# Performance work log

Hardware: AMD Instinct MI355X
Metric: run time of the kernel (lower is better)

## Reference

```python
import jax, jax.numpy as jnp
import numpy as np

N = 1024          # num_nodes
E = 16384         # num_edges (avg degree 16)
D = 256           # in_channels
P = 2.0           # PairwiseDistance p
SELF_ADD = 0.5
UPPER_BOUND = 2.0
# scores lie in [SELF_ADD, 1+SELF_ADD] = [0.5, 1.5], so the greedy loop adds
# at most ceil(UPPER_BOUND / 0.5) = 4 edges; 6 masked steps is a safe bound.
MAX_STEPS = 6


def setup_inputs() -> dict:
    key = jax.random.key(0)
    k1, k2 = jax.random.split(key)
    x = jax.random.normal(k1, (N, D), dtype=jnp.float32)
    edge_index = jax.random.randint(k2, (2, E), 0, N, dtype=jnp.int64)
    return {"x": x, "edge_index": edge_index}


def _edge_scores(x, src, dst):
    # compute_distance_score: L2 pairwise distance, min-max normalized, + self_add
    diff = x[src] - x[dst]                      # [E, D]
    dist = jnp.sqrt(jnp.sum(diff * diff, axis=-1))
    dist = (dist - dist.min()) / (dist.max() - dist.min())
    return dist + SELF_ADD                      # [E]


def _search_all(edge_score, src, dst):
    # Vectorized version of node__cluster_search: for each seed node i, greedily
    # add the min-score edge leaving the cluster until total score >= UPPER_BOUND
    # or no frontier edge exists. Fixed-length masked scan == original while-loop.
    def search(i):
        inc = jnp.zeros((N,), bool).at[i].set(True)      # in_cluster mask
        row = jnp.zeros((N,), jnp.float32)               # node_score_matrix row
        tot = jnp.float32(0.0)

        def step(state, _):
            inc, row, tot = state
            valid = inc[src] & ~inc[dst]                 # frontier edges [E]
            active = (tot < UPPER_BOUND) & jnp.any(valid)
            masked = jnp.where(valid, edge_score, jnp.inf)
            e = jnp.argmin(masked)                       # min-score frontier edge
            s = edge_score[e]
            u, v = src[e], dst[e]
            inc2 = inc.at[v].set(True)
            row2 = row.at[u].add(s * 0.5).at[v].add(s * 0.5)
            inc = jnp.where(active, inc2, inc)
            row = jnp.where(active, row2, row)
            tot = jnp.where(active, tot + s, tot)
            return (inc, row, tot), None

        (inc, row, tot), _ = jax.lax.scan(step, (inc, row, tot), None, length=MAX_STEPS)
        return inc.astype(jnp.float32), row

    return jax.vmap(search)(jnp.arange(N))


def _keep_first_unique_rows(assign):
    # np.unique(..., axis=0) dedup, shape-static variant: keep first occurrence of
    # each distinct binary row, zero out duplicates. Double random-hash row compare.
    rng = np.random.default_rng(12345)
    r1 = jnp.asarray(rng.integers(1, 2**20, size=(N,)), dtype=jnp.int32)
    r2 = jnp.asarray(rng.integers(1, 2**20, size=(N,)), dtype=jnp.int32)
    ai = assign.astype(jnp.int32)
    h1, h2 = ai @ r1, ai @ r2
    eq = (h1[:, None] == h1[None, :]) & (h2[:, None] == h2[None, :])  # [N, N]
    dup = jnp.any(jnp.tril(eq, k=-1), axis=1)
    return (~dup).astype(jnp.float32)


def reference(x, edge_index):
    src, dst = edge_index[0], edge_index[1]
    edge_score = _edge_scores(x, src, dst)
    assign, nsm = _search_all(edge_score, src, dst)      # [N, N], [N, N]

    keep = _keep_first_unique_rows(assign)               # [N]
    assign_k = assign * keep[:, None]
    nsm_k = nsm * keep[:, None]

    # dense adjacency (to_dense_adj), pooled adjacency, binarize, drop self-loops
    adj = jnp.zeros((N, N), jnp.float32).at[src, dst].add(1.0)
    adj_new = assign_k @ adj @ assign_k.T
    adj_new = (adj_new > 0).astype(jnp.float32) * (1.0 - jnp.eye(N, dtype=jnp.float32))

    x_new = nsm_k @ x                                    # pooled features [N, D]
    return adj_new, x_new, assign_k, nsm_k
```

## Files before the change

### kernel.cpp

```cpp
#include <hip/hip_runtime.h>
#include <cstdint>

#define NN 1024
#define NE 16384
#define DF 256
#define UB 2.0f
#define MAXSEL 6
#define CAP 128
#define NB2 1024
#define DSTR 16

typedef unsigned long long u64;

__global__ void k_zero(uint4* __restrict__ p) {
    p[blockIdx.x * 256 + threadIdx.x] = make_uint4(0, 0, 0, 0);
}

__global__ void k_dist_build(const float* __restrict__ x, const int* __restrict__ src,
                             const int* __restrict__ dst, int* __restrict__ deg,
                             u64* __restrict__ slots,
                             uint32_t* __restrict__ pmin, uint32_t* __restrict__ pmax) {
    __shared__ uint32_t smin[4], smax[4];
    int t = threadIdx.x;
    int wid = t >> 6, lane = t & 63;
    int c16 = lane & 15;
    int e = blockIdx.x * 16 + wid * 4 + (lane >> 4);
    int u = src[e], v = dst[e];
    const float4* xa = (const float4*)(x + (size_t)u * DF);
    const float4* xb = (const float4*)(x + (size_t)v * DF);
    float4 a0 = xa[c16],      b0 = xb[c16];
    float4 a1 = xa[c16 + 16], b1 = xb[c16 + 16];
    float4 a2 = xa[c16 + 32], b2 = xb[c16 + 32];
    float4 a3 = xa[c16 + 48], b3 = xb[c16 + 48];
    double s = 0.0;
    {
        float d;
        d = a0.x-b0.x; s += (double)d*d;  d = a0.y-b0.y; s += (double)d*d;
        d = a0.z-b0.z; s += (double)d*d;  d = a0.w-b0.w; s += (double)d*d;
        d = a1.x-b1.x; s += (double)d*d;  d = a1.y-b1.y; s += (double)d*d;
        d = a1.z-b1.z; s += (double)d*d;  d = a1.w-b1.w; s += (double)d*d;
        d = a2.x-b2.x; s += (double)d*d;  d = a2.y-b2.y; s += (double)d*d;
        d = a2.z-b2.z; s += (double)d*d;  d = a2.w-b2.w; s += (double)d*d;
        d = a3.x-b3.x; s += (double)d*d;  d = a3.y-b3.y; s += (double)d*d;
        d = a3.z-b3.z; s += (double)d*d;  d = a3.w-b3.w; s += (double)d*d;
    }
    s += __shfl_xor(s, 1, 64);
    s += __shfl_xor(s, 2, 64);
    s += __shfl_xor(s, 4, 64);
    s += __shfl_xor(s, 8, 64);
    uint32_t db = __float_as_uint(sqrtf((float)s));
    if (c16 == 0) {
        int pos = atomicAdd(&deg[u * DSTR], 1);
        if (pos < CAP)
            slots[(size_t)u * CAP + pos] =
                ((u64)db << 24) | ((u64)(uint32_t)e << 10) | (u64)(uint32_t)v;
    }
    uint32_t mnv = db, mxv = db;
    uint32_t o;
    o = (uint32_t)__shfl_xor((int)mnv, 16, 64); mnv = min(mnv, o);
    o = (uint32_t)__shfl_xor((int)mnv, 32, 64); mnv = min(mnv, o);
    o = (uint32_t)__shfl_xor((int)mxv, 16, 64); mxv = max(mxv, o);
    o = (uint32_t)__shfl_xor((int)mxv, 32, 64); mxv = max(mxv, o);
    if (lane == 0) { smin[wid] = mnv; smax[wid] = mxv; }
    __syncthreads();
    if (t == 0) {
        pmin[blockIdx.x] = min(min(smin[0], smin[1]), min(smin[2], smin[3]));
        pmax[blockIdx.x] = max(max(smax[0], smax[1]), max(smax[2], smax[3]));
    }
}

__global__ void k_search(const int* __restrict__ deg, const u64* __restrict__ slots,
                         const uint32_t* __restrict__ pmin, const uint32_t* __restrict__ pmax,
                         const int* __restrict__ src,
                         uint32_t* __restrict__ masks, uint32_t* __restrict__ maskT,
                         int* __restrict__ selU, int* __restrict__ selV,
                         float* __restrict__ selS, int* __restrict__ selCnt,
                         u64* __restrict__ sig, u64* __restrict__ dc64) {
    __shared__ uint32_t inc[32];
    __shared__ int members[8];
    __shared__ int degL[8], offL[9];
    __shared__ float s_tot;
    __shared__ int s_nmem;
    int i = blockIdx.x, lane = threadIdx.x;
    if (lane < 32) inc[lane] = 0;

    uint32_t mnb = 0xFFFFFFFFu, mxb = 0u;
    const uint4* p4n = (const uint4*)pmin;
    const uint4* p4x = (const uint4*)pmax;
    for (int k = lane; k < NB2 / 4; k += 64) {
        uint4 a = p4n[k], b = p4x[k];
        mnb = min(mnb, min(min(a.x, a.y), min(a.z, a.w)));
        mxb = max(mxb, max(max(b.x, b.y), max(b.z, b.w)));
    }
    for (int off = 32; off; off >>= 1) {
        uint32_t oa = (uint32_t)__shfl_xor((int)mnb, off, 64);
        uint32_t ob = (uint32_t)__shfl_xor((int)mxb, off, 64);
        mnb = min(mnb, oa);
        mxb = max(mxb, ob);
    }
    float MN = __uint_as_float(mnb);
    float MX = __uint_as_float(mxb);

    if (lane == 0) {
        inc[i >> 5] = 1u << (i & 31);
        members[0] = i;
        s_tot = 0.0f;
        s_nmem = 1;
    }
    __syncthreads();
    int cnt = 0;
    for (int step = 0; step < MAXSEL; ++step) {
        if (s_tot >= UB) break;
        int nm = s_nmem;
        if (lane < nm) degL[lane] = min(deg[members[lane] * DSTR], CAP);
        __syncthreads();
        if (lane == 0) {
            offL[0] = 0;
            for (int m = 0; m < nm; ++m) offL[m + 1] = offL[m] + degL[m];
        }
        __syncthreads();
        int T = offL[nm];
        u64 best = ~0ull;
        for (int f = lane; f < T; f += 64) {
            int m = 0;
            while (f >= offL[m + 1]) ++m;
            u64 en = slots[(size_t)members[m] * CAP + (f - offL[m])];
            int v = (int)(en & 1023);
            if (!((inc[v >> 5] >> (v & 31)) & 1u) && en < best) best = en;
        }
        for (int off = 32; off; off >>= 1) {
            u64 o = __shfl_xor(best, off, 64);
            if (o < best) best = o;
        }
        if (best == ~0ull) break;
        if (lane == 0) {
            uint32_t db = (uint32_t)(best >> 24);
            int e = (int)((best >> 10) & 0x3FFF);
            int v = (int)(best & 1023);
            float dd = __uint_as_float(db);
            float s = (dd - MN) / (MX - MN) + 0.5f;
            int u = src[e];
            inc[v >> 5] |= 1u << (v & 31);
            members[s_nmem++] = v;
            selU[i * 8 + cnt] = u;
            selV[i * 8 + cnt] = v;
            selS[i * 8 + cnt] = s;
            s_tot += s;
        }
        cnt++;
        __syncthreads();
    }
    __syncthreads();
    if (lane == 0) {
        selCnt[i] = cnt;
        u64 h = 1469598103934665603ull;
        for (int w = 0; w < 32; ++w) { h ^= inc[w]; h *= 1099511628211ull; }
        sig[i] = h;
        u64 d = 0; int nc = 0;
        for (int k = 1; k < s_nmem; ++k) {
            int v = members[k];
            if (v < i) { d |= ((u64)(uint32_t)v) << (4 + 10 * nc); ++nc; }
        }
        dc64[i] = d | (u64)nc;
    }
    if (lane < 32) masks[(size_t)i * 32 + lane] = inc[lane];
    if (lane < s_nmem) {
        int n = members[lane];
        atomicOr(&maskT[(size_t)n * 32 + (i >> 5)], 1u << (i & 31));
    }
}

__global__ void k_rows(const float* __restrict__ x, const int* __restrict__ deg,
                       const u64* __restrict__ slots,
                       const uint32_t* __restrict__ masks, const uint32_t* __restrict__ maskT,
                       const u64* __restrict__ sig, const u64* __restrict__ dc64,
                       const int* __restrict__ selU, const int* __restrict__ selV,
                       const float* __restrict__ selS, const int* __restrict__ selCnt,
                       float* __restrict__ outAdj, float* __restrict__ outAs,
                       float* __restrict__ outNsm, float* __restrict__ outX) {
    __shared__ u64 sigL[NN];
    __shared__ uint32_t keepb[32];
    __shared__ uint32_t R[32], MI[32], orow[32];
    __shared__ uint32_t part[8][32];
    __shared__ int su[8], ssv[8];
    __shared__ float ss[8];
    __shared__ int s_c;
    int i = blockIdx.x, t = threadIdx.x;

    for (int j = t; j < NN; j += 256) sigL[j] = sig[j];
    if (t < 32) { keepb[t] = 0; R[t] = 0; MI[t] = masks[(size_t)i * 32 + t]; }
    if (t == 0) s_c = selCnt[i];
    if (t < 8) { su[t] = selU[i*8+t]; ssv[t] = selV[i*8+t]; ss[t] = selS[i*8+t]; }
    __syncthreads();

    for (int q = 0; q < 4; ++q) {
        int j = t + q * 256;
        u64 d = dc64[j];
        int cj = (int)(d & 15);
        u64 sj = sigL[j];
        bool dup = false;
        for (int k = 0; k < cj; ++k) {
            int v = (int)((d >> (4 + 10 * k)) & 1023);
            if (sigL[v] == sj) { dup = true; break; }
        }
        if (!dup) atomicOr(&keepb[j >> 5], 1u << (j & 31));
    }

    int c = s_c;
    for (int m = 0; m <= c; ++m) {
        int u = (m == 0) ? i : ssv[m - 1];
        int dc = min(deg[u * DSTR], CAP);
        const u64* sl = slots + (size_t)u * CAP;
        for (int k = t; k < dc; k += 256) {
            int v = (int)(sl[k] & 1023);
            atomicOr(&R[v >> 5], 1u << (v & 31));
        }
    }
    __syncthreads();
    int kp = (keepb[i >> 5] >> (i & 31)) & 1;

    int g = t >> 5, l = t & 31;
    uint32_t acc = 0;
    if (kp) {
        for (int wi = g; wi < 32; wi += 8) {
            uint32_t bits = R[wi];
            while (bits) {
                int b0 = __ffs(bits) - 1; bits &= bits - 1;
                uint32_t v0 = maskT[((size_t)(wi * 32 + b0)) * 32 + l];
                if (bits) {
                    int b1 = __ffs(bits) - 1; bits &= bits - 1;
                    v0 |= maskT[((size_t)(wi * 32 + b1)) * 32 + l];
                }
                acc |= v0;
            }
        }
    }
    part[g][l] = acc;
    __syncthreads();
    if (t < 32) {
        uint32_t o = 0;
        for (int gg = 0; gg < 8; ++gg) o |= part[gg][t];
        orow[t] = o & keepb[t];
    }
    __syncthreads();

    int j0 = t * 4;
    int w = j0 >> 5, sh = j0 & 31;
    float4 vadj = {0,0,0,0}, vas = {0,0,0,0}, vnsm = {0,0,0,0};
    if (kp) {
        uint32_t ob = orow[w] >> sh;
        uint32_t mb = MI[w] >> sh;
        vadj.x = ((ob     ) & 1) && (j0     != i) ? 1.0f : 0.0f;
        vadj.y = ((ob >> 1) & 1) && (j0 + 1 != i) ? 1.0f : 0.0f;
        vadj.z = ((ob >> 2) & 1) && (j0 + 2 != i) ? 1.0f : 0.0f;
        vadj.w = ((ob >> 3) & 1) && (j0 + 3 != i) ? 1.0f : 0.0f;
        vas.x = (mb      & 1) ? 1.0f : 0.0f;
        vas.y = ((mb>>1) & 1) ? 1.0f : 0.0f;
        vas.z = ((mb>>2) & 1) ? 1.0f : 0.0f;
        vas.w = ((mb>>3) & 1) ? 1.0f : 0.0f;
        for (int k = 0; k < c; ++k) {
            float h = ss[k] * 0.5f;
            int u = su[k], v = ssv[k];
            vnsm.x += ((u == j0    ) ? h : 0.0f) + ((v == j0    ) ? h : 0.0f);
            vnsm.y += ((u == j0 + 1) ? h : 0.0f) + ((v == j0 + 1) ? h : 0.0f);
            vnsm.z += ((u == j0 + 2) ? h : 0.0f) + ((v == j0 + 2) ? h : 0.0f);
            vnsm.w += ((u == j0 + 3) ? h : 0.0f) + ((v == j0 + 3) ? h : 0.0f);
        }
    }
    ((float4*)outAdj)[(size_t)i * (NN/4) + t] = vadj;
    ((float4*)outAs )[(size_t)i * (NN/4) + t] = vas;
    ((float4*)outNsm)[(size_t)i * (NN/4) + t] = vnsm;

    float accx = 0.0f;
    if (kp) {
        for (int k = 0; k < c; ++k) {
            float h = ss[k] * 0.5f;
            accx += h * x[(size_t)su[k] * DF + t];
            accx += h * x[(size_t)ssv[k] * DF + t];
        }
    }
    outX[(size_t)i * DF + t] = accx;
}

extern "C" void kernel_launch(void* const* d_in, const int* in_sizes, int n_in,
                              void* d_out, int out_size, void* d_ws, size_t ws_size,
                              hipStream_t stream) {
    const float* x = (const float*)d_in[0];
    const int* ei = (const int*)d_in[1];
    const int* src = ei;
    const int* dst = ei + NE;

    float* out = (float*)d_out;
    float* out_adj = out;
    float* out_x   = out + (size_t)NN * NN;
    float* out_as  = out_x + (size_t)NN * DF;
    float* out_nsm = out_as + (size_t)NN * NN;

    char* w = (char*)d_ws;
    u64*      slots = (u64*)w;       w += (size_t)NN * CAP * 8;
    u64*      sig   = (u64*)w;       w += (size_t)NN * 8;
    u64*      dc64  = (u64*)w;       w += (size_t)NN * 8;
    int*      deg   = (int*)w;       w += (size_t)NN * DSTR * 4;
    uint32_t* maskT = (uint32_t*)w;  w += (size_t)NN * 32 * 4;
    uint32_t* pmin  = (uint32_t*)w;  w += (size_t)NB2 * 4;
    uint32_t* pmax  = (uint32_t*)w;  w += (size_t)NB2 * 4;
    uint32_t* masks = (uint32_t*)w;  w += (size_t)NN * 32 * 4;
    int*      selU  = (int*)w;       w += (size_t)NN * 8 * 4;
    int*      selV  = (int*)w;       w += (size_t)NN * 8 * 4;
    float*    selS  = (float*)w;     w += (size_t)NN * 8 * 4;
    int*      selCnt= (int*)w;       w += (size_t)NN * 4;

    k_zero<<<48, 256, 0, stream>>>((uint4*)deg);
    k_dist_build<<<NB2, 256, 0, stream>>>(x, src, dst, deg, slots, pmin, pmax);
    k_search<<<NN, 64, 0, stream>>>(deg, slots, pmin, pmax, src,
                                    masks, maskT, selU, selV, selS, selCnt, sig, dc64);
    k_rows<<<NN, 256, 0, stream>>>(x, deg, slots, masks, maskT, sig, dc64,
                                   selU, selV, selS, selCnt,
                                   out_adj, out_as, out_nsm, out_x);
}
```

Before: 34.86 us.

## Use sentinel-filled fixed-width adjacency slots and cache member edges in shared memory

Adjacency slot capacity is halved and the slots are pre-filled with all-ones sentinels, so readers scan a fixed 64 entries per node and no longer need per-node degree reads or prefix offsets. The search kernel loads each newly added member's slot row once into a shared-memory pool and rescans it each step, dropping repeated global loads and two barriers per step. The rows kernel builds a compact list of reachable nodes before OR-ing maskT rows. The fill kernel now writes the whole slots array, and any node with more than 64 out-edges would silently lose edges, which is fine for average degree 16 but not guaranteed.

```diff
diff --git a/kernel.cpp b/kernel.cpp
--- a/kernel.cpp
+++ b/kernel.cpp
@@ -6,14 +6,16 @@
 #define DF 256
 #define UB 2.0f
 #define MAXSEL 6
-#define CAP 128
+#define CAP 64
 #define NB2 1024
 #define DSTR 16
+#define FILLB 176
 
 typedef unsigned long long u64;
 
-__global__ void k_zero(uint4* __restrict__ p) {
-    p[blockIdx.x * 256 + threadIdx.x] = make_uint4(0, 0, 0, 0);
+__global__ void k_fill(uint4* __restrict__ p) {
+    uint32_t v = (blockIdx.x < 128) ? 0xFFFFFFFFu : 0u;
+    p[blockIdx.x * 256 + threadIdx.x] = make_uint4(v, v, v, v);
 }
 
 __global__ void k_dist_build(const float* __restrict__ x, const int* __restrict__ src,
@@ -69,16 +71,16 @@
     }
 }
 
-__global__ void k_search(const int* __restrict__ deg, const u64* __restrict__ slots,
+__global__ void k_search(const u64* __restrict__ slots,
                          const uint32_t* __restrict__ pmin, const uint32_t* __restrict__ pmax,
                          const int* __restrict__ src,
                          uint32_t* __restrict__ masks, uint32_t* __restrict__ maskT,
                          int* __restrict__ selU, int* __restrict__ selV,
                          float* __restrict__ selS, int* __restrict__ selCnt,
                          u64* __restrict__ sig, u64* __restrict__ dc64) {
+    __shared__ u64 pool[8][64];
     __shared__ uint32_t inc[32];
     __shared__ int members[8];
-    __shared__ int degL[8], offL[9];
     __shared__ float s_tot;
     __shared__ int s_nmem;
     int i = blockIdx.x, lane = threadIdx.x;
@@ -107,26 +109,20 @@
         s_tot = 0.0f;
         s_nmem = 1;
     }
+    pool[0][lane] = slots[(size_t)i * CAP + lane];
     __syncthreads();
     int cnt = 0;
     for (int step = 0; step < MAXSEL; ++step) {
         if (s_tot >= UB) break;
         int nm = s_nmem;
-        if (lane < nm) degL[lane] = min(deg[members[lane] * DSTR], CAP);
-        __syncthreads();
-        if (lane == 0) {
-            offL[0] = 0;
-            for (int m = 0; m < nm; ++m) offL[m + 1] = offL[m] + degL[m];
-        }
-        __syncthreads();
-        int T = offL[nm];
         u64 best = ~0ull;
-        for (int f = lane; f < T; f += 64) {
-            int m = 0;
-            while (f >= offL[m + 1]) ++m;
-            u64 en = slots[(size_t)members[m] * CAP + (f - offL[m])];
-            int v = (int)(en & 1023);
-            if (!((inc[v >> 5] >> (v & 31)) & 1u) && en < best) best = en;
+        #pragma unroll
+        for (int m = 0; m < 8; ++m) {
+            if (m < nm) {
+                u64 en = pool[m][lane];
+                int v = (int)(en & 1023);
+                if (!((inc[v >> 5] >> (v & 31)) & 1u) && en < best) best = en;
+            }
         }
         for (int off = 32; off; off >>= 1) {
             u64 o = __shfl_xor(best, off, 64);
@@ -139,15 +135,17 @@
             int v = (int)(best & 1023);
             float dd = __uint_as_float(db);
             float s = (dd - MN) / (MX - MN) + 0.5f;
-            int u = src[e];
             inc[v >> 5] |= 1u << (v & 31);
             members[s_nmem++] = v;
-            selU[i * 8 + cnt] = u;
+            selU[i * 8 + cnt] = src[e];
             selV[i * 8 + cnt] = v;
             selS[i * 8 + cnt] = s;
             s_tot += s;
         }
         cnt++;
+        __syncthreads();
+        int newm = s_nmem - 1;
+        pool[newm][lane] = slots[(size_t)members[newm] * CAP + lane];
         __syncthreads();
     }
     __syncthreads();
@@ -170,8 +168,7 @@
     }
 }
 
-__global__ void k_rows(const float* __restrict__ x, const int* __restrict__ deg,
-                       const u64* __restrict__ slots,
+__global__ void k_rows(const float* __restrict__ x, const u64* __restrict__ slots,
                        const uint32_t* __restrict__ masks, const uint32_t* __restrict__ maskT,
                        const u64* __restrict__ sig, const u64* __restrict__ dc64,
                        const int* __restrict__ selU, const int* __restrict__ selV,
@@ -182,6 +179,8 @@
     __shared__ uint32_t keepb[32];
     __shared__ uint32_t R[32], MI[32], orow[32];
     __shared__ uint32_t part[8][32];
+    __shared__ int list[512];
+    __shared__ int s_lcnt;
     __shared__ int su[8], ssv[8];
     __shared__ float ss[8];
     __shared__ int s_c;
@@ -189,7 +188,7 @@
 
     for (int j = t; j < NN; j += 256) sigL[j] = sig[j];
     if (t < 32) { keepb[t] = 0; R[t] = 0; MI[t] = masks[(size_t)i * 32 + t]; }
-    if (t == 0) s_c = selCnt[i];
+    if (t == 0) { s_c = selCnt[i]; s_lcnt = 0; }
     if (t < 8) { su[t] = selU[i*8+t]; ssv[t] = selV[i*8+t]; ss[t] = selS[i*8+t]; }
     __syncthreads();
 
@@ -207,33 +206,36 @@
     }
 
     int c = s_c;
-    for (int m = 0; m <= c; ++m) {
+    int total = (c + 1) * CAP;
+    for (int k = t; k < total; k += 256) {
+        int m = k >> 6;
         int u = (m == 0) ? i : ssv[m - 1];
-        int dc = min(deg[u * DSTR], CAP);
-        const u64* sl = slots + (size_t)u * CAP;
-        for (int k = t; k < dc; k += 256) {
-            int v = (int)(sl[k] & 1023);
+        u64 en = slots[(size_t)u * CAP + (k & 63)];
+        if (en != ~0ull) {
+            int v = (int)(en & 1023);
             atomicOr(&R[v >> 5], 1u << (v & 31));
         }
     }
     __syncthreads();
     int kp = (keepb[i >> 5] >> (i & 31)) & 1;
+
+    if (t < 32) {
+        uint32_t bits = R[t];
+        while (bits) {
+            int b = __ffs(bits) - 1;
+            bits &= bits - 1;
+            int p = atomicAdd(&s_lcnt, 1);
+            list[p] = t * 32 + b;
+        }
+    }
+    __syncthreads();
+    int lcnt = s_lcnt;
 
     int g = t >> 5, l = t & 31;
     uint32_t acc = 0;
     if (kp) {
-        for (int wi = g; wi < 32; wi += 8) {
-            uint32_t bits = R[wi];
-            while (bits) {
-                int b0 = __ffs(bits) - 1; bits &= bits - 1;
-                uint32_t v0 = maskT[((size_t)(wi * 32 + b0)) * 32 + l];
-                if (bits) {
-                    int b1 = __ffs(bits) - 1; bits &= bits - 1;
-                    v0 |= maskT[((size_t)(wi * 32 + b1)) * 32 + l];
-                }
-                acc |= v0;
-            }
-        }
+        for (int k = g; k < lcnt; k += 8)
+            acc |= maskT[(size_t)list[k] * 32 + l];
     }
     part[g][l] = acc;
     __syncthreads();
@@ -298,10 +300,10 @@
 
     char* w = (char*)d_ws;
     u64*      slots = (u64*)w;       w += (size_t)NN * CAP * 8;
+    int*      deg   = (int*)w;       w += (size_t)NN * DSTR * 4;
+    uint32_t* maskT = (uint32_t*)w;  w += (size_t)NN * 32 * 4;
     u64*      sig   = (u64*)w;       w += (size_t)NN * 8;
     u64*      dc64  = (u64*)w;       w += (size_t)NN * 8;
-    int*      deg   = (int*)w;       w += (size_t)NN * DSTR * 4;
-    uint32_t* maskT = (uint32_t*)w;  w += (size_t)NN * 32 * 4;
     uint32_t* pmin  = (uint32_t*)w;  w += (size_t)NB2 * 4;
     uint32_t* pmax  = (uint32_t*)w;  w += (size_t)NB2 * 4;
     uint32_t* masks = (uint32_t*)w;  w += (size_t)NN * 32 * 4;
@@ -310,11 +312,11 @@
     float*    selS  = (float*)w;     w += (size_t)NN * 8 * 4;
     int*      selCnt= (int*)w;       w += (size_t)NN * 4;
 
-    k_zero<<<48, 256, 0, stream>>>((uint4*)deg);
+    k_fill<<<FILLB, 256, 0, stream>>>((uint4*)slots);
     k_dist_build<<<NB2, 256, 0, stream>>>(x, src, dst, deg, slots, pmin, pmax);
-    k_search<<<NN, 64, 0, stream>>>(deg, slots, pmin, pmax, src,
+    k_search<<<NN, 64, 0, stream>>>(slots, pmin, pmax, src,
                                     masks, maskT, selU, selV, selS, selCnt, sig, dc64);
-    k_rows<<<NN, 256, 0, stream>>>(x, deg, slots, masks, maskT, sig, dc64,
+    k_rows<<<NN, 256, 0, stream>>>(x, slots, masks, maskT, sig, dc64,
                                    selU, selV, selS, selCnt,
                                    out_adj, out_as, out_nsm, out_x);
 }
```

New measurement: 33.77 us. -3.1%, faster.
